# Optimization experiments

Hardware: AMD Instinct MI355X
Metric: run time of the kernel (lower is better)

## Reference

```python
import jax, jax.numpy as jnp
import numpy as np

B, S, D = 2, 2048, 1024
H = 16
HD = D // H  # head_dim = 64


def setup_inputs() -> dict:
    key = jax.random.key(0)
    ks = jax.random.split(key, 6)
    scale = 0.02
    x = jax.random.normal(ks[0], (B, S, D), dtype=jnp.float32)
    Wq = jax.random.normal(ks[1], (D, D), dtype=jnp.float32) * scale
    Wk = jax.random.normal(ks[2], (D, D), dtype=jnp.float32) * scale
    Wv = jax.random.normal(ks[3], (D, D), dtype=jnp.float32) * scale
    Wo = jax.random.normal(ks[4], (D, D), dtype=jnp.float32) * scale
    bo = jax.random.normal(ks[5], (D,), dtype=jnp.float32) * scale
    return {"x": x, "Wq": Wq, "Wk": Wk, "Wv": Wv, "Wo": Wo, "bo": bo}


def reference(x, Wq, Wk, Wv, Wo, bo):
    b, s, d = x.shape
    # QKV projections (no bias, qkv_bias=False)
    Q = (x @ Wq).reshape(b, s, H, HD)
    K = (x @ Wk).reshape(b, s, H, HD)
    V = (x @ Wv).reshape(b, s, H, HD)
    # [b, h, q, k] attention scores
    scores = jnp.einsum('bqhd,bkhd->bhqk', Q, K)
    # causal mask: positions k > q masked to -inf (applied before scaling, as in source;
    # -inf / sqrt(hd) is still -inf so this matches)
    causal = jnp.triu(jnp.ones((s, s), dtype=bool), k=1)
    scores = jnp.where(causal, -jnp.inf, scores)
    att = jax.nn.softmax(scores / jnp.sqrt(jnp.float32(HD)), axis=-1)
    # dropout p=0.0 -> identity
    ctx = jnp.einsum('bhqk,bkhd->bqhd', att, V).reshape(b, s, d)
    return ctx @ Wo + bo
```

## Files before the change

### kernel.cpp

```cpp
#include <hip/hip_runtime.h>

typedef __bf16 bf16;
typedef __attribute__((ext_vector_type(8))) __bf16 bf16x8;
typedef __attribute__((ext_vector_type(4))) __bf16 bf16x4;
typedef __attribute__((ext_vector_type(4))) float floatx4;

#define MFMA16(a, b, c) __builtin_amdgcn_mfma_f32_16x16x32_bf16((a), (b), (c), 0, 0, 0)

static constexpr int BB = 2, SS = 2048, DD = 1024, HH = 16;
static constexpr int MM = BB * SS;
static constexpr int N_QKV = 3 * DD;

__device__ __forceinline__ float exp2c(float x) {
#if __has_builtin(__builtin_amdgcn_exp2f)
    return __builtin_amdgcn_exp2f(x);
#else
    return exp2f(x);
#endif
}

__device__ __forceinline__ void async16(const void* g, void* l) {
    __builtin_amdgcn_global_load_lds(
        (const __attribute__((address_space(1))) unsigned int*)g,
        (__attribute__((address_space(3))) unsigned int*)l, 16, 0, 0);
}

__global__ __launch_bounds__(256) void cvt_x_kernel(const float* __restrict__ x,
                                                    bf16* __restrict__ xb) {
    int i = (blockIdx.x * 256 + threadIdx.x) * 4;
    float4 v = *(const float4*)(x + i);
    bf16x4 o;
    o[0] = (bf16)v.x; o[1] = (bf16)v.y; o[2] = (bf16)v.z; o[3] = (bf16)v.w;
    *(bf16x4*)(xb + i) = o;
}

__global__ __launch_bounds__(256) void cvt_wT_kernel(const float* __restrict__ w0,
                                                     const float* __restrict__ w1,
                                                     const float* __restrict__ w2,
                                                     const float* __restrict__ w3,
                                                     bf16* __restrict__ outT) {
    __shared__ float tile[32][33];
    const float* src = (blockIdx.z == 0) ? w0 : (blockIdx.z == 1) ? w1
                      : (blockIdx.z == 2) ? w2 : w3;
    bf16* dst = outT + (size_t)blockIdx.z * DD * DD;
    int x = blockIdx.x * 32 + threadIdx.x;
    int y0 = blockIdx.y * 32;
    for (int i = threadIdx.y; i < 32; i += 8)
        tile[i][threadIdx.x] = src[(size_t)(y0 + i) * DD + x];
    __syncthreads();
    int xo = y0 + threadIdx.x;
    int yo0 = blockIdx.x * 32;
    for (int i = threadIdx.y; i < 32; i += 8)
        dst[(size_t)(yo0 + i) * DD + xo] = (bf16)tile[threadIdx.x][i];
}

__global__ __launch_bounds__(256) void transpose_v_kernel(const bf16* __restrict__ QKV,
                                                          bf16* __restrict__ Vt_g) {
    __shared__ bf16 t[64][72];
    const int tid = threadIdx.x, srow = tid >> 2, sseg = tid & 3;
    const int bh = blockIdx.y, b = bh >> 4, h = bh & 15;
    const int s0 = blockIdx.x * 64;
    {
        const uint4* p = (const uint4*)(QKV + (size_t)(b * SS + s0 + srow) * N_QKV
                                        + 2 * DD + h * 64 + sseg * 16);
        uint4 a = p[0], c = p[1];
        uint4* d = (uint4*)&t[srow][sseg * 16];
        d[0] = a; d[1] = c;
    }
    __syncthreads();
    bf16x8 o0, o1;
#pragma unroll
    for (int e = 0; e < 8; ++e) o0[e] = t[sseg * 16 + e][srow];
#pragma unroll
    for (int e = 0; e < 8; ++e) o1[e] = t[sseg * 16 + 8 + e][srow];
    uint4* d = (uint4*)(Vt_g + ((size_t)bh * 64 + srow) * SS + s0 + sseg * 16);
    d[0] = *(uint4*)&o0; d[1] = *(uint4*)&o1;
}

template <int BM, int BN, bool OUT_BF16>
__global__ __launch_bounds__(256) void gemm_kernel(const bf16* __restrict__ A,
                                                   const bf16* __restrict__ Bt,
                                                   void* __restrict__ C,
                                                   const float* __restrict__ bias,
                                                   int K, int ldc) {
    constexpr int MT = BM / 32, NT = BN / 32;
    __shared__ bf16 As[BM * 64];
    __shared__ bf16 Bs[BN * 64];
    const int tid = threadIdx.x, wave = tid >> 6, lane = tid & 63;
    const int quad = lane >> 4, l16 = lane & 15;
    const int wm = wave >> 1, wn = wave & 1;
    const int m0 = blockIdx.y * BM, n0 = blockIdx.x * BN;
    const int l8r = lane >> 3, l8c = lane & 7;
    const int gch = ((l8c ^ l8r) * 8);

    floatx4 acc[MT][NT] = {};

    for (int k0 = 0; k0 < K; k0 += 64) {
        __syncthreads();
#pragma unroll
        for (int c = 0; c < BM / 32; ++c) {
            int r = wave * (BM / 4) + c * 8;
            async16(A + (size_t)(m0 + r + l8r) * K + k0 + gch, &As[r * 64]);
        }
#pragma unroll
        for (int c = 0; c < BN / 32; ++c) {
            int r = wave * (BN / 4) + c * 8;
            async16(Bt + (size_t)(n0 + r + l8r) * K + k0 + gch, &Bs[r * 64]);
        }
        __syncthreads();
#pragma unroll
        for (int cc = 0; cc < 2; ++cc) {
            bf16x8 af[MT], bv[NT];
#pragma unroll
            for (int i = 0; i < MT; ++i) {
                int row = wm * (BM / 2) + i * 16 + l16;
                af[i] = *(const bf16x8*)&As[row * 64 + ((cc * 4 + quad) ^ (row & 7)) * 8];
            }
#pragma unroll
            for (int j = 0; j < NT; ++j) {
                int row = wn * (BN / 2) + j * 16 + l16;
                bv[j] = *(const bf16x8*)&Bs[row * 64 + ((cc * 4 + quad) ^ (row & 7)) * 8];
            }
#pragma unroll
            for (int i = 0; i < MT; ++i)
#pragma unroll
                for (int j = 0; j < NT; ++j)
                    acc[i][j] = MFMA16(af[i], bv[j], acc[i][j]);
        }
    }

#pragma unroll
    for (int i = 0; i < MT; ++i)
#pragma unroll
        for (int j = 0; j < NT; ++j)
#pragma unroll
            for (int r = 0; r < 4; ++r) {
                int row = m0 + wm * (BM / 2) + i * 16 + quad * 4 + r;
                int col = n0 + wn * (BN / 2) + j * 16 + l16;
                if (OUT_BF16)
                    ((bf16*)C)[(size_t)row * ldc + col] = (bf16)acc[i][j][r];
                else
                    ((float*)C)[(size_t)row * ldc + col] = acc[i][j][r] + bias[col];
            }
}

__global__ __launch_bounds__(256) void attn_kernel(const bf16* __restrict__ QKV,
                                                   const bf16* __restrict__ Vt_g,
                                                   bf16* __restrict__ ctx) {
    __shared__ bf16 Qs[64][72];
    __shared__ bf16 Ks[2][64][72];
    __shared__ bf16 Vt[2][64][72];
    __shared__ bf16 Ps[4][16][72];

    const int tid = threadIdx.x, wave = tid >> 6, lane = tid & 63;
    const int quad = lane >> 4, l16 = lane & 15;
    const int g = blockIdx.x;
    const int xcd = g & 7, rr = g >> 3;
    const int bh = xcd * 4 + (rr & 3), qp = rr >> 2;
    const int b = bh >> 4, h = bh & 15;
    const int srow = tid >> 2, sseg = tid & 3;
    const size_t base = (size_t)(b * SS) * N_QKV;
    const bf16* Vg = Vt_g + (size_t)bh * 64 * SS;
    constexpr float C2 = 0.18033688011112042f;

    bf16x8 onesf = {};
    if (l16 == 0) {
#pragma unroll
        for (int e = 0; e < 8; ++e) onesf[e] = (bf16)1.0f;
    }

    for (int half = 0; half < 2; ++half) {
        const int qt = half ? (31 - qp) : qp;
        const int q0 = qt * 64;

        {
            const uint4* pq = (const uint4*)(QKV + base + (size_t)(q0 + srow) * N_QKV
                                             + h * 64 + sseg * 16);
            uint4 a = pq[0], bq = pq[1];
            uint4* d = (uint4*)&Qs[srow][sseg * 16];
            d[0] = a; d[1] = bq;
        }
        uint4 kr0, kr1, vr0, vr1;
        {
            const uint4* pk = (const uint4*)(QKV + base + (size_t)srow * N_QKV
                                             + DD + h * 64 + sseg * 16);
            kr0 = pk[0]; kr1 = pk[1];
            const uint4* pv = (const uint4*)(Vg + (size_t)srow * SS + sseg * 16);
            vr0 = pv[0]; vr1 = pv[1];
        }
        __syncthreads();

        const bf16x8 qf0 = *(const bf16x8*)&Qs[wave * 16 + l16][quad * 8];
        const bf16x8 qf1 = *(const bf16x8*)&Qs[wave * 16 + l16][32 + quad * 8];
        const int qg = q0 + wave * 16 + l16;

        floatx4 accv[4] = {};
        floatx4 acc5 = {};
        float m_run = -__builtin_inff();

        for (int kt = 0; kt <= qt; ++kt) {
            const int buf = kt & 1;
            {
                uint4* dk = (uint4*)&Ks[buf][srow][sseg * 16];
                dk[0] = kr0; dk[1] = kr1;
                uint4* dv = (uint4*)&Vt[buf][srow][sseg * 16];
                dv[0] = vr0; dv[1] = vr1;
            }
            __syncthreads();
            if (kt < qt) {
                int k0n = (kt + 1) * 64;
                const uint4* pk = (const uint4*)(QKV + base + (size_t)(k0n + srow) * N_QKV
                                                 + DD + h * 64 + sseg * 16);
                kr0 = pk[0]; kr1 = pk[1];
                const uint4* pv = (const uint4*)(Vg + (size_t)srow * SS + k0n + sseg * 16);
                vr0 = pv[0]; vr1 = pv[1];
            }
            const int k0 = kt * 64;

            floatx4 st[4];
#pragma unroll
            for (int j = 0; j < 4; ++j) {
                bf16x8 kf0 = *(const bf16x8*)&Ks[buf][j * 16 + l16][quad * 8];
                bf16x8 kf1 = *(const bf16x8*)&Ks[buf][j * 16 + l16][32 + quad * 8];
                floatx4 t = {};
                t = MFMA16(kf0, qf0, t);
                t = MFMA16(kf1, qf1, t);
                st[j] = t;
            }

#pragma unroll
            for (int j = 0; j < 4; ++j) {
                int kb = k0 + j * 16 + quad * 4;
#pragma unroll
                for (int r = 0; r < 4; ++r)
                    if (kb + r > qg) st[j][r] = -__builtin_inff();
            }

            float mloc = fmaxf(fmaxf(st[0][0], st[0][1]), fmaxf(st[0][2], st[0][3]));
#pragma unroll
            for (int j = 1; j < 4; ++j)
                mloc = fmaxf(mloc, fmaxf(fmaxf(st[j][0], st[j][1]),
                                         fmaxf(st[j][2], st[j][3])));
            mloc = fmaxf(mloc, __shfl_xor(mloc, 16, 64));
            mloc = fmaxf(mloc, __shfl_xor(mloc, 32, 64));

            const float m_new = fmaxf(m_run, mloc);
            const float alpha = exp2c((m_run - m_new) * C2);
            const float mm = m_new * C2;
            m_run = m_new;

#pragma unroll
            for (int j = 0; j < 4; ++j) {
                bf16x4 pk;
#pragma unroll
                for (int r = 0; r < 4; ++r) {
                    float p = exp2c(fmaf(st[j][r], C2, -mm));
                    pk[r] = (bf16)p;
                }
                *(bf16x4*)&Ps[wave][l16][j * 16 + quad * 4] = pk;
            }

            const int bsrc = (lane & 48) | ((lane >> 2) & 12);
            float ar[4];
#pragma unroll
            for (int r = 0; r < 4; ++r) ar[r] = __shfl(alpha, bsrc + r, 64);
#pragma unroll
            for (int j = 0; j < 4; ++j)
#pragma unroll
                for (int r = 0; r < 4; ++r) accv[j][r] *= ar[r];
#pragma unroll
            for (int r = 0; r < 4; ++r) acc5[r] *= ar[r];

            bf16x8 pf0 = *(const bf16x8*)&Ps[wave][l16][quad * 8];
            bf16x8 pf1 = *(const bf16x8*)&Ps[wave][l16][32 + quad * 8];
#pragma unroll
            for (int j = 0; j < 4; ++j) {
                bf16x8 vt0 = *(const bf16x8*)&Vt[buf][j * 16 + l16][quad * 8];
                bf16x8 vt1 = *(const bf16x8*)&Vt[buf][j * 16 + l16][32 + quad * 8];
                accv[j] = MFMA16(pf0, vt0, accv[j]);
                accv[j] = MFMA16(pf1, vt1, accv[j]);
            }
            acc5 = MFMA16(pf0, onesf, acc5);
            acc5 = MFMA16(pf1, onesf, acc5);
        }

        float inv[4];
#pragma unroll
        for (int r = 0; r < 4; ++r) {
            float lr = __shfl(acc5[r], lane & 48, 64);
            inv[r] = 1.0f / lr;
        }
#pragma unroll
        for (int j = 0; j < 4; ++j)
#pragma unroll
            for (int r = 0; r < 4; ++r) {
                int row = b * SS + q0 + wave * 16 + quad * 4 + r;
                int col = h * 64 + j * 16 + l16;
                ctx[(size_t)row * DD + col] = (bf16)(accv[j][r] * inv[r]);
            }
    }
}

extern "C" void kernel_launch(void* const* d_in, const int* in_sizes, int n_in,
                              void* d_out, int out_size, void* d_ws, size_t ws_size,
                              hipStream_t stream) {
    const float* x  = (const float*)d_in[0];
    const float* Wq = (const float*)d_in[1];
    const float* Wk = (const float*)d_in[2];
    const float* Wv = (const float*)d_in[3];
    const float* Wo = (const float*)d_in[4];
    const float* bo = (const float*)d_in[5];
    float* out = (float*)d_out;

    char* ws = (char*)d_ws;
    bf16* xb   = (bf16*)ws;
    bf16* WT   = (bf16*)(ws + (size_t)(8  << 20));
    bf16* QKV  = (bf16*)(ws + (size_t)(16 << 20));
    bf16* ctxb = (bf16*)(ws + (size_t)(40 << 20));
    bf16* Vt_g = (bf16*)(ws + (size_t)(48 << 20));

    cvt_x_kernel<<<dim3(MM * DD / (256 * 4)), dim3(256), 0, stream>>>(x, xb);
    cvt_wT_kernel<<<dim3(32, 32, 4), dim3(32, 8), 0, stream>>>(Wq, Wk, Wv, Wo, WT);
    gemm_kernel<128, 128, true><<<dim3(N_QKV / 128, MM / 128), dim3(256), 0, stream>>>(
        xb, WT, QKV, nullptr, DD, N_QKV);
    transpose_v_kernel<<<dim3(SS / 64, BB * HH), dim3(256), 0, stream>>>(QKV, Vt_g);
    attn_kernel<<<dim3(512), dim3(256), 0, stream>>>(QKV, Vt_g, ctxb);
    gemm_kernel<128, 64, false><<<dim3(DD / 64, MM / 128), dim3(256), 0, stream>>>(
        ctxb, WT + (size_t)3 * DD * DD, out, bo, DD, DD);
}
```

Before: 189.4 us.

## Enlarge attention query tile to 128 rows with XOR-swizzled shared memory

After: 191.3 us. No clear change (+1.0%).

```diff
diff --git a/kernel.cpp b/kernel.cpp
--- a/kernel.cpp
+++ b/kernel.cpp
@@ -144,159 +144,190 @@
             }
 }
 
-__global__ __launch_bounds__(256) void attn_kernel(const bf16* __restrict__ QKV,
-                                                   const bf16* __restrict__ Vt_g,
-                                                   bf16* __restrict__ ctx) {
-    __shared__ bf16 Qs[64][72];
-    __shared__ bf16 Ks[2][64][72];
-    __shared__ bf16 Vt[2][64][72];
-    __shared__ bf16 Ps[4][16][72];
+__global__ __launch_bounds__(256, 2) void attn_kernel(const bf16* __restrict__ QKV,
+                                                      const bf16* __restrict__ Vt_g,
+                                                      bf16* __restrict__ ctx) {
+    __shared__ __align__(16) bf16 smem[24576];
+    bf16* Ks = smem;
+    bf16* Vt = smem + 8192;
+    bf16* Ps = smem + 16384;
+    bf16* Qs = smem;
 
     const int tid = threadIdx.x, wave = tid >> 6, lane = tid & 63;
     const int quad = lane >> 4, l16 = lane & 15;
-    const int g = blockIdx.x;
-    const int xcd = g & 7, rr = g >> 3;
-    const int bh = xcd * 4 + (rr & 3), qp = rr >> 2;
+    const int gb = blockIdx.x;
+    const int xcd = gb & 7, rr = gb >> 3;
+    int bhl, t;
+    if (rr < 32) { bhl = rr >> 4;              t = rr & 15; }
+    else         { bhl = 2 + ((rr & 31) >> 4); t = 15 - (rr & 15); }
+    const int bh = xcd * 4 + bhl;
     const int b = bh >> 4, h = bh & 15;
+    const int q0 = t * 128;
     const int srow = tid >> 2, sseg = tid & 3;
     const size_t base = (size_t)(b * SS) * N_QKV;
     const bf16* Vg = Vt_g + (size_t)bh * 64 * SS;
     constexpr float C2 = 0.18033688011112042f;
 
+    uint4 kr0, kr1, vr0, vr1;
+    {
+        const uint4* pk = (const uint4*)(QKV + base + (size_t)srow * N_QKV + DD + h * 64 + sseg * 16);
+        kr0 = pk[0]; kr1 = pk[1];
+        const uint4* pv = (const uint4*)(Vg + (size_t)srow * SS + sseg * 16);
+        vr0 = pv[0]; vr1 = pv[1];
+    }
+    {
+        const int l8r = lane >> 3, l8c = lane & 7;
+#pragma unroll
+        for (int c = 0; c < 4; ++c) {
+            int r0 = wave * 32 + c * 8;
+            async16(QKV + base + (size_t)(q0 + r0 + l8r) * N_QKV + h * 64 + (l8c ^ l8r) * 8,
+                    Qs + r0 * 64);
+        }
+    }
+    __syncthreads();
+    bf16x8 qf[2][2];
+#pragma unroll
+    for (int gg = 0; gg < 2; ++gg)
+#pragma unroll
+        for (int cc = 0; cc < 2; ++cc) {
+            int row = wave * 32 + gg * 16 + l16;
+            qf[gg][cc] = *(const bf16x8*)&Qs[row * 64 + ((cc * 4 + quad) ^ (l16 & 7)) * 8];
+        }
+    __syncthreads();
+
     bf16x8 onesf = {};
     if (l16 == 0) {
 #pragma unroll
         for (int e = 0; e < 8; ++e) onesf[e] = (bf16)1.0f;
     }
 
-    for (int half = 0; half < 2; ++half) {
-        const int qt = half ? (31 - qp) : qp;
-        const int q0 = qt * 64;
-
+    floatx4 accv[2][4] = {};
+    floatx4 acc5[2] = {};
+    float m_run[2] = { -__builtin_inff(), -__builtin_inff() };
+    const int qg0 = q0 + wave * 32 + l16;
+    const int bsrc = (lane & 48) | ((lane >> 2) & 12);
+    const int nkt = 2 * t + 2;
+    const int swz = (l16 & 7);
+
+    for (int kt = 0; kt < nkt; ++kt) {
+        const int buf = kt & 1;
         {
-            const uint4* pq = (const uint4*)(QKV + base + (size_t)(q0 + srow) * N_QKV
-                                             + h * 64 + sseg * 16);
-            uint4 a = pq[0], bq = pq[1];
-            uint4* d = (uint4*)&Qs[srow][sseg * 16];
-            d[0] = a; d[1] = bq;
-        }
-        uint4 kr0, kr1, vr0, vr1;
-        {
-            const uint4* pk = (const uint4*)(QKV + base + (size_t)srow * N_QKV
+            const int p0 = (2 * sseg) ^ (srow & 7), p1 = (2 * sseg + 1) ^ (srow & 7);
+            *(uint4*)&Ks[buf * 4096 + srow * 64 + p0 * 8] = kr0;
+            *(uint4*)&Ks[buf * 4096 + srow * 64 + p1 * 8] = kr1;
+            *(uint4*)&Vt[buf * 4096 + srow * 64 + p0 * 8] = vr0;
+            *(uint4*)&Vt[buf * 4096 + srow * 64 + p1 * 8] = vr1;
+        }
+        __syncthreads();
+        if (kt + 1 < nkt) {
+            int k0n = (kt + 1) * 64;
+            const uint4* pk = (const uint4*)(QKV + base + (size_t)(k0n + srow) * N_QKV
                                              + DD + h * 64 + sseg * 16);
             kr0 = pk[0]; kr1 = pk[1];
-            const uint4* pv = (const uint4*)(Vg + (size_t)srow * SS + sseg * 16);
+            const uint4* pv = (const uint4*)(Vg + (size_t)srow * SS + k0n + sseg * 16);
             vr0 = pv[0]; vr1 = pv[1];
         }
-        __syncthreads();
-
-        const bf16x8 qf0 = *(const bf16x8*)&Qs[wave * 16 + l16][quad * 8];
-        const bf16x8 qf1 = *(const bf16x8*)&Qs[wave * 16 + l16][32 + quad * 8];
-        const int qg = q0 + wave * 16 + l16;
-
-        floatx4 accv[4] = {};
-        floatx4 acc5 = {};
-        float m_run = -__builtin_inff();
-
-        for (int kt = 0; kt <= qt; ++kt) {
-            const int buf = kt & 1;
-            {
-                uint4* dk = (uint4*)&Ks[buf][srow][sseg * 16];
-                dk[0] = kr0; dk[1] = kr1;
-                uint4* dv = (uint4*)&Vt[buf][srow][sseg * 16];
-                dv[0] = vr0; dv[1] = vr1;
-            }
-            __syncthreads();
-            if (kt < qt) {
-                int k0n = (kt + 1) * 64;
-                const uint4* pk = (const uint4*)(QKV + base + (size_t)(k0n + srow) * N_QKV
-                                                 + DD + h * 64 + sseg * 16);
-                kr0 = pk[0]; kr1 = pk[1];
-                const uint4* pv = (const uint4*)(Vg + (size_t)srow * SS + k0n + sseg * 16);
-                vr0 = pv[0]; vr1 = pv[1];
-            }
-            const int k0 = kt * 64;
-
-            floatx4 st[4];
+        const int k0 = kt * 64;
+
+        floatx4 st[2][4];
+#pragma unroll
+        for (int j = 0; j < 4; ++j) { st[0][j] = (floatx4){}; st[1][j] = (floatx4){}; }
+#pragma unroll
+        for (int cc = 0; cc < 2; ++cc)
 #pragma unroll
             for (int j = 0; j < 4; ++j) {
-                bf16x8 kf0 = *(const bf16x8*)&Ks[buf][j * 16 + l16][quad * 8];
-                bf16x8 kf1 = *(const bf16x8*)&Ks[buf][j * 16 + l16][32 + quad * 8];
-                floatx4 t = {};
-                t = MFMA16(kf0, qf0, t);
-                t = MFMA16(kf1, qf1, t);
-                st[j] = t;
-            }
-
-#pragma unroll
-            for (int j = 0; j < 4; ++j) {
-                int kb = k0 + j * 16 + quad * 4;
-#pragma unroll
-                for (int r = 0; r < 4; ++r)
-                    if (kb + r > qg) st[j][r] = -__builtin_inff();
-            }
-
-            float mloc = fmaxf(fmaxf(st[0][0], st[0][1]), fmaxf(st[0][2], st[0][3]));
+                bf16x8 kf = *(const bf16x8*)&Ks[buf * 4096 + (j * 16 + l16) * 64
+                                                + ((cc * 4 + quad) ^ swz) * 8];
+                st[0][j] = MFMA16(kf, qf[0][cc], st[0][j]);
+                st[1][j] = MFMA16(kf, qf[1][cc], st[1][j]);
+            }
+
+        if (64 * kt + 63 > q0 + 32 * wave) {
+#pragma unroll
+            for (int gg = 0; gg < 2; ++gg) {
+                const int qq = qg0 + gg * 16;
+#pragma unroll
+                for (int j = 0; j < 4; ++j) {
+                    int kb = k0 + j * 16 + quad * 4;
+#pragma unroll
+                    for (int r = 0; r < 4; ++r)
+                        if (kb + r > qq) st[gg][j][r] = -__builtin_inff();
+                }
+            }
+        }
+
+#pragma unroll
+        for (int gg = 0; gg < 2; ++gg) {
+            float mloc = fmaxf(fmaxf(st[gg][0][0], st[gg][0][1]),
+                               fmaxf(st[gg][0][2], st[gg][0][3]));
 #pragma unroll
             for (int j = 1; j < 4; ++j)
-                mloc = fmaxf(mloc, fmaxf(fmaxf(st[j][0], st[j][1]),
-                                         fmaxf(st[j][2], st[j][3])));
+                mloc = fmaxf(mloc, fmaxf(fmaxf(st[gg][j][0], st[gg][j][1]),
+                                         fmaxf(st[gg][j][2], st[gg][j][3])));
             mloc = fmaxf(mloc, __shfl_xor(mloc, 16, 64));
             mloc = fmaxf(mloc, __shfl_xor(mloc, 32, 64));
 
-            const float m_new = fmaxf(m_run, mloc);
-            const float alpha = exp2c((m_run - m_new) * C2);
+            const float m_new = fmaxf(m_run[gg], mloc);
+            const float alpha = exp2c((m_run[gg] - m_new) * C2);
             const float mm = m_new * C2;
-            m_run = m_new;
+            m_run[gg] = m_new;
 
 #pragma unroll
             for (int j = 0; j < 4; ++j) {
-                bf16x4 pk;
-#pragma unroll
-                for (int r = 0; r < 4; ++r) {
-                    float p = exp2c(fmaf(st[j][r], C2, -mm));
-                    pk[r] = (bf16)p;
-                }
-                *(bf16x4*)&Ps[wave][l16][j * 16 + quad * 4] = pk;
-            }
-
-            const int bsrc = (lane & 48) | ((lane >> 2) & 12);
+                bf16x4 pk4;
+#pragma unroll
+                for (int r = 0; r < 4; ++r)
+                    pk4[r] = (bf16)exp2c(fmaf(st[gg][j][r], C2, -mm));
+                *(bf16x4*)&Ps[wave * 2048 + gg * 1024 + l16 * 64
+                              + ((2 * j + (quad >> 1)) ^ swz) * 8 + (quad & 1) * 4] = pk4;
+            }
+
             float ar[4];
 #pragma unroll
             for (int r = 0; r < 4; ++r) ar[r] = __shfl(alpha, bsrc + r, 64);
 #pragma unroll
             for (int j = 0; j < 4; ++j)
 #pragma unroll
-                for (int r = 0; r < 4; ++r) accv[j][r] *= ar[r];
-#pragma unroll
-            for (int r = 0; r < 4; ++r) acc5[r] *= ar[r];
-
-            bf16x8 pf0 = *(const bf16x8*)&Ps[wave][l16][quad * 8];
-            bf16x8 pf1 = *(const bf16x8*)&Ps[wave][l16][32 + quad * 8];
+                for (int r = 0; r < 4; ++r) accv[gg][j][r] *= ar[r];
+#pragma unroll
+            for (int r = 0; r < 4; ++r) acc5[gg][r] *= ar[r];
+        }
+
+        bf16x8 pf[2][2];
+#pragma unroll
+        for (int gg = 0; gg < 2; ++gg)
+#pragma unroll
+            for (int cc = 0; cc < 2; ++cc)
+                pf[gg][cc] = *(const bf16x8*)&Ps[wave * 2048 + gg * 1024 + l16 * 64
+                                                 + ((cc * 4 + quad) ^ swz) * 8];
+#pragma unroll
+        for (int cc = 0; cc < 2; ++cc)
 #pragma unroll
             for (int j = 0; j < 4; ++j) {
-                bf16x8 vt0 = *(const bf16x8*)&Vt[buf][j * 16 + l16][quad * 8];
-                bf16x8 vt1 = *(const bf16x8*)&Vt[buf][j * 16 + l16][32 + quad * 8];
-                accv[j] = MFMA16(pf0, vt0, accv[j]);
-                accv[j] = MFMA16(pf1, vt1, accv[j]);
-            }
-            acc5 = MFMA16(pf0, onesf, acc5);
-            acc5 = MFMA16(pf1, onesf, acc5);
-        }
-
+                bf16x8 vt = *(const bf16x8*)&Vt[buf * 4096 + (j * 16 + l16) * 64
+                                                + ((cc * 4 + quad) ^ swz) * 8];
+                accv[0][j] = MFMA16(pf[0][cc], vt, accv[0][j]);
+                accv[1][j] = MFMA16(pf[1][cc], vt, accv[1][j]);
+            }
+        acc5[0] = MFMA16(pf[0][0], onesf, acc5[0]);
+        acc5[0] = MFMA16(pf[0][1], onesf, acc5[0]);
+        acc5[1] = MFMA16(pf[1][0], onesf, acc5[1]);
+        acc5[1] = MFMA16(pf[1][1], onesf, acc5[1]);
+    }
+
+#pragma unroll
+    for (int gg = 0; gg < 2; ++gg) {
         float inv[4];
 #pragma unroll
-        for (int r = 0; r < 4; ++r) {
-            float lr = __shfl(acc5[r], lane & 48, 64);
-            inv[r] = 1.0f / lr;
-        }
+        for (int r = 0; r < 4; ++r)
+            inv[r] = 1.0f / __shfl(acc5[gg][r], lane & 48, 64);
 #pragma unroll
         for (int j = 0; j < 4; ++j)
 #pragma unroll
             for (int r = 0; r < 4; ++r) {
-                int row = b * SS + q0 + wave * 16 + quad * 4 + r;
+                int row = b * SS + q0 + wave * 32 + gg * 16 + quad * 4 + r;
                 int col = h * 64 + j * 16 + l16;
-                ctx[(size_t)row * DD + col] = (bf16)(accv[j][r] * inv[r]);
+                ctx[(size_t)row * DD + col] = (bf16)(accv[gg][j][r] * inv[r]);
             }
     }
 }
```
